# Performance work log

Measured on AMD Instinct MI355X. Metric: run time of the kernel, lower is better.

Reference implementation:

```python
import jax, jax.numpy as jnp
import numpy as np

N = 50000        # num nodes
E = 800000       # num edges (avg degree 16)
IN = 64          # in_channels
H = 128          # hidden_channels
C1 = 64          # Num_TCN (fine clusters)
C2 = 16          # Num_TCN2 (coarse clusters)
DROP = 0.5       # drop_rate
THRESH = 1.0 / (C1 - 1)  # default edge_pruning_threshold
LN_EPS = 1e-5


def layer_norm(x, g, b):
    mu = jnp.mean(x, axis=-1, keepdims=True)
    var = jnp.var(x, axis=-1, keepdims=True)
    return (x - mu) * jax.lax.rsqrt(var + LN_EPS) * g + b


def graph_conv(x_src, row, col, W_rel, b, W_root, num_nodes):
    # PyG GraphConv (aggr='add'): out = lin_rel(sum_{src->dst} x[src]) + lin_root(x)
    agg = jax.ops.segment_sum(x_src[row], col, num_segments=num_nodes)
    return agg @ W_rel.T + b + x_src @ W_root.T


def mincut_common(x, s, A_s, deg):
    # shared tail of sparse_mincut_pool given A_s = A @ s and degree vector
    C = s.shape[-1]
    pooled_x = s.T @ x                                   # [C, F]
    pooled_adj = s.T @ A_s                               # [C, C]
    mincut_num = jnp.trace(pooled_adj)
    mincut_den = jnp.trace(s.T @ (deg[:, None] * s)) + 1e-10
    mincut_loss = -mincut_num / mincut_den
    sTs = s.T @ s
    norm = jnp.linalg.norm(sTs)
    ortho_loss = jnp.linalg.norm(sTs / (norm + 1e-10) - jnp.eye(C, dtype=x.dtype) / jnp.sqrt(jnp.asarray(C, x.dtype)))
    adj = pooled_adj * (1.0 - jnp.eye(C, dtype=x.dtype))  # fill_diagonal_(0)
    d_sqrt_inv = 1.0 / (jnp.sqrt(adj.sum(axis=1)) + 1e-15)
    adj_norm = adj * d_sqrt_inv[:, None] * d_sqrt_inv[None, :]
    return pooled_x, adj_norm, mincut_loss, ortho_loss


def mincut_sparse(x, row, col, s_logits, num_nodes):
    s = jax.nn.softmax(s_logits, axis=-1)
    # A_s[row] += s[col]  (edge_weight = 1) -> [N, C] scatter-add
    A_s = jax.ops.segment_sum(s[col], row, num_segments=num_nodes)
    deg = jax.ops.segment_sum(jnp.ones((row.shape[0],), x.dtype), row, num_segments=num_nodes)
    return mincut_common(x, s, A_s, deg)


def mincut_dense(x, M, s_logits):
    # pooled graph: dense 0/1 adjacency M[i,j]; equivalent to edge list from nonzero(M)
    s = jax.nn.softmax(s_logits, axis=-1)
    A_s = M @ s
    deg = M.sum(axis=1)
    return mincut_common(x, s, A_s, deg)


def setup_inputs() -> dict:
    key = jax.random.key(0)
    ks = jax.random.split(key, 12)
    x = jax.random.normal(ks[0], (N, IN), jnp.float32)
    edge_index = jax.random.randint(ks[1], (2, E), 0, N, jnp.int32)
    # bernoulli(1 - drop_rate) node-drop mask, fixed for determinism
    drop_mask = (jax.random.uniform(ks[2], (N,)) > DROP).astype(jnp.float32)
    p = lambda k, shp: (jax.random.normal(k, shp, jnp.float32) * 0.05)
    return dict(
        x=x, edge_index=edge_index, drop_mask=drop_mask,
        W1_rel=p(ks[3], (H, IN)), b1=jnp.zeros((H,), jnp.float32), W1_root=p(ks[4], (H, IN)),
        pW1=p(ks[5], (C1, H)), pb1=jnp.zeros((C1,), jnp.float32),
        g1=jnp.ones((C1,), jnp.float32), be1=jnp.zeros((C1,), jnp.float32),
        W2_rel=p(ks[6], (H, H)), b2=jnp.zeros((H,), jnp.float32), W2_root=p(ks[7], (H, H)),
        pW2=p(ks[8], (C2, H)), pb2=jnp.zeros((C2,), jnp.float32),
        g2=jnp.ones((C2,), jnp.float32), be2=jnp.zeros((C2,), jnp.float32),
    )


def reference(x, edge_index, drop_mask, W1_rel, b1, W1_root, pW1, pb1, g1, be1,
              W2_rel, b2, W2_root, pW2, pb2, g2, be2):
    # training=True path, S=1 (loss sums / S are identity)
    row, col = edge_index[0], edge_index[1]
    x_drop = drop_mask[:, None] * x
    x1 = jax.nn.relu(graph_conv(x_drop, row, col, W1_rel, b1, W1_root, N))   # [N, H]
    s1 = layer_norm(x1 @ pW1.T + pb1, g1, be1)                               # [N, C1]
    ls1 = jax.nn.log_softmax(s1, axis=-1)
    x_pool1, adj_pool1, mc1, o1 = mincut_sparse(x1, row, col, s1, N)
    # edge pruning -> dense 0/1 pooled adjacency (replaces nonzero + edge list)
    M = jnp.where(adj_pool1 > THRESH, 1.0, 0.0).astype(x.dtype)              # [C1, C1]
    # GraphConv on pooled graph: aggregate x[src] at dst == M.T @ x_pool1
    x2 = jax.nn.relu((M.T @ x_pool1) @ W2_rel.T + b2 + x_pool1 @ W2_root.T)  # [C1, H]
    s2 = layer_norm(x2 @ pW2.T + pb2, g2, be2)                               # [C1, C2]
    ls2 = jax.nn.log_softmax(s2, axis=-1)
    _, _, mc2, o2 = mincut_dense(x2, M, s2)
    return (mc1, o1, mc2, o2, ls1, ls2)
```

## Files before the change

kernel.cpp:

```cpp
#include <hip/hip_runtime.h>
#include <hip/hip_bf16.h>
#include <hip/hip_fp16.h>

#define NN 50000
#define NE 800000
#define INC 64
#define HC 128
#define NC1 64
#define NC2 16
#define DCAP 64

#define OFF_FLAG 0
#define OFW_W1R 16
#define OFW_W1O 8208
#define OFW_B1  16400
#define OFW_PW1 16528
#define OFW_PB1 24720
#define OFW_G1  24784
#define OFW_BE1 24848
#define OFW_W2R 24912
#define OFW_B2  41296
#define OFW_W2O 41424
#define OFW_PW2 57808
#define OFW_PB2 59856
#define OFW_G2  59872
#define OFW_BE2 59888
#define CVT_TOTAL 59888

#define OFW_PW1T 59904
#define OFF_MG   68096
#define OFF_MTG  72192
#define OFF_DEG2 76288
#define OFF_S2G  76352
#define OFW_WCT  77376
#define OFF_XD   127792
#define OFF_X1   3327792
#define OFF_S    9727792
#define OFF_AGG  12927792
#define OFF_CSRC 16127792
#define OFF_SCAL 17727792
#define OFF_PX   17727808
#define OFF_PADJ 17736000
#define OFF_STS  17740096
#define OFF_CUR  17744192
#define OFF_Q    17794192
#define OFF_END  17844192
#define ZERO_FLOATS (OFF_END - OFF_SCAL)

#define OFF_PXSTSP OFF_XD
#define OFF_PADJP  OFF_X1
#define OFF_XD16   OFF_X1
#define OFF_S16    OFF_AGG
#define P_POOL 256
#define P_PADJ 1536
#define XSS 132

#define FC_G 2048
#define FC_SLICES (FC_G >> 3)
#define FC_ES ((NE + FC_SLICES - 1) / FC_SLICES)
#define FC_RANGE (NN >> 3)

__device__ inline float bflo(unsigned int u){ return __uint_as_float(u << 16); }
__device__ inline float bfhi(unsigned int u){ return __uint_as_float(u & 0xffff0000u); }

__device__ inline void store_out(void* out, long long idx, float v, bool bf){
  if (bf) ((__hip_bfloat16*)out)[idx] = __float2bfloat16(v);
  else    ((float*)out)[idx] = v;
}

__device__ inline float block_reduce_256(float v, float* red, int t){
  red[t] = v; __syncthreads();
#pragma unroll
  for (int sh = 128; sh > 0; sh >>= 1){
    if (t < sh) red[t] += red[t + sh];
    __syncthreads();
  }
  float r = red[0];
  __syncthreads();
  return r;
}

__global__ void k_detect(const unsigned int* __restrict__ dmw, float* __restrict__ flag){
  __shared__ int cnt;
  if (threadIdx.x == 0) cnt = 0;
  __syncthreads();
  int c = 0;
  for (int i = threadIdx.x; i < 12288; i += 256){
    unsigned int w = dmw[i];
    if (w == 0x3F803F80u || w == 0x00003F80u) c++;
  }
  atomicAdd(&cnt, c);
  __syncthreads();
  if (threadIdx.x == 0) flag[0] = (cnt > 64) ? 1.0f : 0.0f;
}

__global__ void k_cvt(const void* p0, const void* p1, const void* p2, const void* p3,
                      const void* p4, const void* p5, const void* p6, const void* p7,
                      const void* p8, const void* p9, const void* p10, const void* p11,
                      const void* p12, const void* p13,
                      const float* __restrict__ flag, float* __restrict__ ws){
  int i = blockIdx.x * blockDim.x + threadIdx.x;
  if (i >= CVT_TOTAL) return;
  const void* src; int off;
  if      (i < 8192 ){ src = p0;  off = i; }
  else if (i < 16384){ src = p1;  off = i - 8192; }
  else if (i < 16512){ src = p2;  off = i - 16384; }
  else if (i < 24704){ src = p3;  off = i - 16512; }
  else if (i < 24768){ src = p4;  off = i - 24704; }
  else if (i < 24832){ src = p5;  off = i - 24768; }
  else if (i < 24896){ src = p6;  off = i - 24832; }
  else if (i < 41280){ src = p7;  off = i - 24896; }
  else if (i < 41408){ src = p8;  off = i - 41280; }
  else if (i < 57792){ src = p9;  off = i - 41408; }
  else if (i < 59840){ src = p10; off = i - 57792; }
  else if (i < 59856){ src = p11; off = i - 59840; }
  else if (i < 59872){ src = p12; off = i - 59856; }
  else               { src = p13; off = i - 59872; }
  float v = (flag[0] > 0.5f) ? __bfloat162float(((const __hip_bfloat16*)src)[off])
                             : ((const float*)src)[off];
  ws[16 + i] = v;
  if (i < 8192){
    int h = i >> 6, j = i & 63;
    ws[OFW_WCT + j * 128 + h] = v;
  } else if (i < 16384){
    int o2 = i - 8192;
    int h = o2 >> 6, j = o2 & 63;
    ws[OFW_WCT + (64 + j) * 128 + h] = v;
  } else if (i >= 16512 && i < 24704){
    int o2 = i - 16512;
    int c = o2 >> 7, k = o2 & 127;
    ws[OFW_PW1T + k * 64 + c] = v;
  }
}

__global__ void k_xdrop(const void* __restrict__ xr, const void* __restrict__ dmr,
                        const float* __restrict__ flag, float* __restrict__ xd,
                        __half* __restrict__ xd16){
  int i4 = blockIdx.x * blockDim.x + threadIdx.x;
  if (i4 >= NN * 16) return;
  int n = i4 >> 4;
  float4 o;
  if (flag[0] > 0.5f){
    uint2 w = ((const uint2*)xr)[i4];
    float dv = __bfloat162float(((const __hip_bfloat16*)dmr)[n]);
    o.x = bflo(w.x) * dv; o.y = bfhi(w.x) * dv;
    o.z = bflo(w.y) * dv; o.w = bfhi(w.y) * dv;
  } else {
    float4 xv = ((const float4*)xr)[i4];
    float dv = ((const float*)dmr)[n];
    o.x = xv.x * dv; o.y = xv.y * dv; o.z = xv.z * dv; o.w = xv.w * dv;
  }
  ((float4*)xd)[i4] = o;
  __half2 ha = __floats2half2_rn(o.x, o.y);
  __half2 hb = __floats2half2_rn(o.z, o.w);
  uint2 hh;
  hh.x = *(unsigned int*)&ha;
  hh.y = *(unsigned int*)&hb;
  ((uint2*)xd16)[i4] = hh;
}

__global__ __launch_bounds__(256) void k_fillC(const int* __restrict__ ei, int* __restrict__ cur,
                        unsigned short* __restrict__ csrc2){
  int p = blockIdx.x & 7;
  int q = blockIdx.x >> 3;
  int lo = p * FC_RANGE;
  int base = q * FC_ES;
  int end = base + FC_ES; if (end > NE) end = NE;
  for (int e = base + (int)threadIdx.x; e < end; e += 256){
    int c = ei[NE + e];
    if ((unsigned)(c - lo) < (unsigned)FC_RANGE){
      int r = ei[e];
      int pos = atomicAdd(&cur[c], 1);
      if (pos < DCAP) csrc2[(c << 6) + pos] = (unsigned short)r;
    }
  }
}

#define G4ACC(Sq, Cq, Aq) \
    if (slot < Cq){ \
      uint2 u = *(const uint2*)(table + (Sq << 6) + (sub << 2)); \
      float2 f0 = __half22float2(*(__half2*)&u.x); \
      float2 f1 = __half22float2(*(__half2*)&u.y); \
      Aq.x += f0.x; Aq.y += f0.y; Aq.z += f1.x; Aq.w += f1.y; \
    }

__device__ inline void gather4h(const unsigned short* __restrict__ idx,
                                const int* __restrict__ cur,
                                int n0, const __half* __restrict__ table,
                                int lane, int g, int sub,
                                float4& A0, float4& A1, float4& A2, float4& A3){
  int c0 = cur[n0 + 0]; if (c0 > DCAP) c0 = DCAP;
  int c1 = cur[n0 + 1]; if (c1 > DCAP) c1 = DCAP;
  int c2 = cur[n0 + 2]; if (c2 > DCAP) c2 = DCAP;
  int c3 = cur[n0 + 3]; if (c3 > DCAP) c3 = DCAP;
  int my0 = (int)idx[((n0 + 0) << 6) + lane];
  int my1 = (int)idx[((n0 + 1) << 6) + lane];
  int my2 = (int)idx[((n0 + 2) << 6) + lane];
  int my3 = (int)idx[((n0 + 3) << 6) + lane];
  A0 = make_float4(0.f, 0.f, 0.f, 0.f); A1 = A0; A2 = A0; A3 = A0;
  int cmax = c0; if (c1 > cmax) cmax = c1; if (c2 > cmax) cmax = c2; if (c3 > cmax) cmax = c3;
#pragma unroll
  for (int i = 0; i < 4; ++i){
    int slot = g + (i << 2);
    int s0 = __shfl(my0, slot, 64);
    int s1 = __shfl(my1, slot, 64);
    int s2 = __shfl(my2, slot, 64);
    int s3 = __shfl(my3, slot, 64);
    G4ACC(s0, c0, A0)
    G4ACC(s1, c1, A1)
    G4ACC(s2, c2, A2)
    G4ACC(s3, c3, A3)
  }
  for (int i = 4; (i << 2) < cmax; ++i){
    int slot = g + (i << 2);
    int s0 = __shfl(my0, slot, 64);
    int s1 = __shfl(my1, slot, 64);
    int s2 = __shfl(my2, slot, 64);
    int s3 = __shfl(my3, slot, 64);
    G4ACC(s0, c0, A0)
    G4ACC(s1, c1, A1)
    G4ACC(s2, c2, A2)
    G4ACC(s3, c3, A3)
  }
}

__device__ inline void red4x(float4& A0, float4& A1, float4& A2, float4& A3){
#pragma unroll
  for (int o = 16; o < 64; o <<= 1){
    A0.x += __shfl_xor(A0.x, o, 64); A0.y += __shfl_xor(A0.y, o, 64);
    A0.z += __shfl_xor(A0.z, o, 64); A0.w += __shfl_xor(A0.w, o, 64);
    A1.x += __shfl_xor(A1.x, o, 64); A1.y += __shfl_xor(A1.y, o, 64);
    A1.z += __shfl_xor(A1.z, o, 64); A1.w += __shfl_xor(A1.w, o, 64);
    A2.x += __shfl_xor(A2.x, o, 64); A2.y += __shfl_xor(A2.y, o, 64);
    A2.z += __shfl_xor(A2.z, o, 64); A2.w += __shfl_xor(A2.w, o, 64);
    A3.x += __shfl_xor(A3.x, o, 64); A3.y += __shfl_xor(A3.y, o, 64);
    A3.z += __shfl_xor(A3.z, o, 64); A3.w += __shfl_xor(A3.w, o, 64);
  }
}

__global__ __launch_bounds__(256) void k_agg2(const int* __restrict__ cur,
                                              const unsigned short* __restrict__ csrc2,
                                              const __half* __restrict__ xd16,
                                              float* __restrict__ agg){
  int gid = blockIdx.x * 256 + threadIdx.x;
  int lane = gid & 63, wid = gid >> 6;
  int nw = (gridDim.x * 256) >> 6;
  int g = lane >> 4, sub = lane & 15;
  for (int nb = wid; nb < (NN >> 2); nb += nw){
    int n0 = nb << 2;
    float4 A0, A1, A2, A3;
    gather4h(csrc2, cur, n0, xd16, lane, g, sub, A0, A1, A2, A3);
    red4x(A0, A1, A2, A3);
    float4 W = (g == 0) ? A0 : (g == 1) ? A1 : (g == 2) ? A2 : A3;
    *(float4*)(agg + ((n0 + g) << 6) + (sub << 2)) = W;
  }
}

#define FMA4(ACC, AV) \
  ACC.x += AV.x*w0.x + AV.y*w1.x + AV.z*w2.x + AV.w*w3.x; \
  ACC.y += AV.x*w0.y + AV.y*w1.y + AV.z*w2.y + AV.w*w3.y; \
  ACC.z += AV.x*w0.z + AV.y*w1.z + AV.z*w2.z + AV.w*w3.z; \
  ACC.w += AV.x*w0.w + AV.y*w1.w + AV.z*w2.w + AV.w*w3.w;

__global__ __launch_bounds__(512, 2) void k_x1(const float* __restrict__ agg,
                                               const float* __restrict__ xd,
                                               const float* __restrict__ wts,
                                               float* __restrict__ x1){
  __shared__ __align__(16) float wt[128 * 128];
  __shared__ __align__(16) float at[64 * 128];
  int t = threadIdx.x;
  for (int f4 = t; f4 < 4096; f4 += 512)
    *(float4*)&wt[f4 << 2] = *(const float4*)&wts[OFW_WCT + (f4 << 2)];
  int ni = t >> 5;
  int cj = t & 31;
  float4 b4 = *(const float4*)&wts[OFW_B1 + (cj << 2)];
  const int ntiles = (NN + 63) >> 6;
  for (int tile = blockIdx.x; tile < ntiles; tile += gridDim.x){
    int base = tile << 6;
    __syncthreads();
    for (int f4 = t; f4 < 2048; f4 += 512){
      int i = f4 >> 5, kq = f4 & 31;
      int n = base + i;
      float4 v = make_float4(0.f, 0.f, 0.f, 0.f);
      if (n < NN){
        int k = kq << 2;
        v = (k < 64) ? *(const float4*)(agg + (n << 6) + k)
                     : *(const float4*)(xd  + (n << 6) + (k - 64));
      }
      *(float4*)&at[(i << 7) + (kq << 2)] = v;
    }
    __syncthreads();
    float4 acc0 = {0,0,0,0}, acc1 = {0,0,0,0}, acc2 = {0,0,0,0}, acc3 = {0,0,0,0};
    const float* ap = at + (ni << 9);
    const float* wp = wt + (cj << 2);
#pragma unroll 4
    for (int k = 0; k < 128; k += 4){
      float4 w0 = *(const float4*)(wp + ((k + 0) << 7));
      float4 w1 = *(const float4*)(wp + ((k + 1) << 7));
      float4 w2 = *(const float4*)(wp + ((k + 2) << 7));
      float4 w3 = *(const float4*)(wp + ((k + 3) << 7));
      float4 a0v = *(const float4*)(ap + k);
      float4 a1v = *(const float4*)(ap + 128 + k);
      float4 a2v = *(const float4*)(ap + 256 + k);
      float4 a3v = *(const float4*)(ap + 384 + k);
      FMA4(acc0, a0v)
      FMA4(acc1, a1v)
      FMA4(acc2, a2v)
      FMA4(acc3, a3v)
    }
    int n0 = base + (ni << 2);
    if (n0 + 0 < NN){
      float4 o; o.x = fmaxf(acc0.x + b4.x, 0.f); o.y = fmaxf(acc0.y + b4.y, 0.f);
      o.z = fmaxf(acc0.z + b4.z, 0.f); o.w = fmaxf(acc0.w + b4.w, 0.f);
      *(float4*)(x1 + (long long)(n0 + 0) * HC + (cj << 2)) = o;
    }
    if (n0 + 1 < NN){
      float4 o; o.x = fmaxf(acc1.x + b4.x, 0.f); o.y = fmaxf(acc1.y + b4.y, 0.f);
      o.z = fmaxf(acc1.z + b4.z, 0.f); o.w = fmaxf(acc1.w + b4.w, 0.f);
      *(float4*)(x1 + (long long)(n0 + 1) * HC + (cj << 2)) = o;
    }
    if (n0 + 2 < NN){
      float4 o; o.x = fmaxf(acc2.x + b4.x, 0.f); o.y = fmaxf(acc2.y + b4.y, 0.f);
      o.z = fmaxf(acc2.z + b4.z, 0.f); o.w = fmaxf(acc2.w + b4.w, 0.f);
      *(float4*)(x1 + (long long)(n0 + 2) * HC + (cj << 2)) = o;
    }
    if (n0 + 3 < NN){
      float4 o; o.x = fmaxf(acc3.x + b4.x, 0.f); o.y = fmaxf(acc3.y + b4.y, 0.f);
      o.z = fmaxf(acc3.z + b4.z, 0.f); o.w = fmaxf(acc3.w + b4.w, 0.f);
      *(float4*)(x1 + (long long)(n0 + 3) * HC + (cj << 2)) = o;
    }
  }
}

__global__ __launch_bounds__(256) void k_s1f(const float* __restrict__ x1,
                                             const float* __restrict__ wts,
                                             float* __restrict__ s,
                                             __half* __restrict__ s16,
                                             float* __restrict__ q,
                                             void* __restrict__ outp,
                                             const float* __restrict__ flag){
  __shared__ float xs[64 * XSS];
  __shared__ float pwc[64 * 64];
  __shared__ float gsh[64], bsh[64];
  int t = threadIdx.x;
  int base = blockIdx.x * 64;
  if (t < 64){ gsh[t] = wts[OFW_G1 + t]; bsh[t] = wts[OFW_BE1 + t]; }
  for (int f = t; f < 64 * 32; f += 256){
    int r = f >> 5, kq = f & 31;
    float4 v = (base + r < NN) ? *(const float4*)(x1 + (base + r) * HC + (kq << 2))
                               : make_float4(0, 0, 0, 0);
    *(float4*)&xs[r * XSS + (kq << 2)] = v;
  }
  int ni = t >> 4, cj = t & 15;
  float4 c0 = {0,0,0,0}, c1 = {0,0,0,0}, c2 = {0,0,0,0}, c3 = {0,0,0,0};
#pragma unroll
  for (int half = 0; half < 2; ++half){
    int k0 = half << 6;
    __syncthreads();
    for (int f = t; f < 1024; f += 256){
      int kk = f >> 4, qq = f & 15;
      *(float4*)&pwc[kk * 64 + (qq << 2)] =
          *(const float4*)&wts[OFW_PW1T + (k0 + kk) * 64 + (qq << 2)];
    }
    __syncthreads();
    for (int kk = 0; kk < 64; kk += 4){
      float4 a0 = *(const float4*)&xs[(ni * 4 + 0) * XSS + k0 + kk];
      float4 a1 = *(const float4*)&xs[(ni * 4 + 1) * XSS + k0 + kk];
      float4 a2 = *(const float4*)&xs[(ni * 4 + 2) * XSS + k0 + kk];
      float4 a3 = *(const float4*)&xs[(ni * 4 + 3) * XSS + k0 + kk];
      float4 b0 = *(const float4*)&pwc[(kk + 0) * 64 + (cj << 2)];
      float4 b1 = *(const float4*)&pwc[(kk + 1) * 64 + (cj << 2)];
      float4 b2 = *(const float4*)&pwc[(kk + 2) * 64 + (cj << 2)];
      float4 b3 = *(const float4*)&pwc[(kk + 3) * 64 + (cj << 2)];
      c0.x += a0.x*b0.x + a0.y*b1.x + a0.z*b2.x + a0.w*b3.x;
      c0.y += a0.x*b0.y + a0.y*b1.y + a0.z*b2.y + a0.w*b3.y;
      c0.z += a0.x*b0.z + a0.y*b1.z + a0.z*b2.z + a0.w*b3.z;
      c0.w += a0.x*b0.w + a0.y*b1.w + a0.z*b2.w + a0.w*b3.w;
      c1.x += a1.x*b0.x + a1.y*b1.x + a1.z*b2.x + a1.w*b3.x;
      c1.y += a1.x*b0.y + a1.y*b1.y + a1.z*b2.y + a1.w*b3.y;
      c1.z += a1.x*b0.z + a1.y*b1.z + a1.z*b2.z + a1.w*b3.z;
      c1.w += a1.x*b0.w + a1.y*b1.w + a1.z*b2.w + a1.w*b3.w;
      c2.x += a2.x*b0.x + a2.y*b1.x + a2.z*b2.x + a2.w*b3.x;
      c2.y += a2.x*b0.y + a2.y*b1.y + a2.z*b2.y + a2.w*b3.y;
      c2.z += a2.x*b0.z + a2.y*b1.z + a2.z*b2.z + a2.w*b3.z;
      c2.w += a2.x*b0.w + a2.y*b1.w + a2.z*b2.w + a2.w*b3.w;
      c3.x += a3.x*b0.x + a3.y*b1.x + a3.z*b2.x + a3.w*b3.x;
      c3.y += a3.x*b0.y + a3.y*b1.y + a3.z*b2.y + a3.w*b3.y;
      c3.z += a3.x*b0.z + a3.y*b1.z + a3.z*b2.z + a3.w*b3.z;
      c3.w += a3.x*b0.w + a3.y*b1.w + a3.z*b2.w + a3.w*b3.w;
    }
  }
  float4 pb = *(const float4*)&wts[OFW_PB1 + (cj << 2)];
  c0.x += pb.x; c0.y += pb.y; c0.z += pb.z; c0.w += pb.w;
  c1.x += pb.x; c1.y += pb.y; c1.z += pb.z; c1.w += pb.w;
  c2.x += pb.x; c2.y += pb.y; c2.z += pb.z; c2.w += pb.w;
  c3.x += pb.x; c3.y += pb.y; c3.z += pb.z; c3.w += pb.w;
  __syncthreads();
  *(float4*)&xs[(ni * 4 + 0) * XSS + (cj << 2)] = c0;
  *(float4*)&xs[(ni * 4 + 1) * XSS + (cj << 2)] = c1;
  *(float4*)&xs[(ni * 4 + 2) * XSS + (cj << 2)] = c2;
  *(float4*)&xs[(ni * 4 + 3) * XSS + (cj << 2)] = c3;
  __syncthreads();
  bool bf = flag[0] > 0.5f;
  int lane = t & 63, wv = t >> 6;
  float gl = gsh[lane], bl = bsh[lane];
  for (int rb = 0; rb < 16; rb += 4){
    int row = wv * 16 + rb;
    float z0 = xs[(row + 0) * XSS + lane];
    float z1 = xs[(row + 1) * XSS + lane];
    float z2 = xs[(row + 2) * XSS + lane];
    float z3 = xs[(row + 3) * XSS + lane];
    float s0 = z0, s1 = z1, s2 = z2, s3 = z3;
    float q0 = z0*z0, q1 = z1*z1, q2 = z2*z2, q3 = z3*z3;
#pragma unroll
    for (int o = 32; o > 0; o >>= 1){
      s0 += __shfl_xor(s0, o, 64); q0 += __shfl_xor(q0, o, 64);
      s1 += __shfl_xor(s1, o, 64); q1 += __shfl_xor(q1, o, 64);
      s2 += __shfl_xor(s2, o, 64); q2 += __shfl_xor(q2, o, 64);
      s3 += __shfl_xor(s3, o, 64); q3 += __shfl_xor(q3, o, 64);
    }
    float mu0 = s0 * 0.015625f, mu1 = s1 * 0.015625f;
    float mu2 = s2 * 0.015625f, mu3 = s3 * 0.015625f;
    float va0 = q0 * 0.015625f - mu0 * mu0;
    float va1 = q1 * 0.015625f - mu1 * mu1;
    float va2 = q2 * 0.015625f - mu2 * mu2;
    float va3 = q3 * 0.015625f - mu3 * mu3;
    float y0 = (z0 - mu0) * rsqrtf(va0 + 1e-5f) * gl + bl;
    float y1 = (z1 - mu1) * rsqrtf(va1 + 1e-5f) * gl + bl;
    float y2 = (z2 - mu2) * rsqrtf(va2 + 1e-5f) * gl + bl;
    float y3 = (z3 - mu3) * rsqrtf(va3 + 1e-5f) * gl + bl;
    float m0 = y0, m1 = y1, m2 = y2, m3 = y3;
#pragma unroll
    for (int o = 32; o > 0; o >>= 1){
      m0 = fmaxf(m0, __shfl_xor(m0, o, 64));
      m1 = fmaxf(m1, __shfl_xor(m1, o, 64));
      m2 = fmaxf(m2, __shfl_xor(m2, o, 64));
      m3 = fmaxf(m3, __shfl_xor(m3, o, 64));
    }
    float e0 = expf(y0 - m0), e1 = expf(y1 - m1);
    float e2 = expf(y2 - m2), e3 = expf(y3 - m3);
    float u0 = e0, u1 = e1, u2 = e2, u3 = e3;
    float w0 = e0*e0, w1 = e1*e1, w2 = e2*e2, w3 = e3*e3;
#pragma unroll
    for (int o = 32; o > 0; o >>= 1){
      u0 += __shfl_xor(u0, o, 64); w0 += __shfl_xor(w0, o, 64);
      u1 += __shfl_xor(u1, o, 64); w1 += __shfl_xor(w1, o, 64);
      u2 += __shfl_xor(u2, o, 64); w2 += __shfl_xor(w2, o, 64);
      u3 += __shfl_xor(u3, o, 64); w3 += __shfl_xor(w3, o, 64);
    }
    int n0 = base + row;
    if (n0 + 0 < NN){ float sv = e0 / u0; s[(n0 + 0) * 64 + lane] = sv;
      s16[(n0 + 0) * 64 + lane] = __float2half(sv);
      store_out(outp, 4LL + (long long)(n0 + 0) * 64 + lane, (y0 - m0) - logf(u0), bf);
      if (lane == 0) q[n0 + 0] = w0 / (u0 * u0); }
    if (n0 + 1 < NN){ float sv = e1 / u1; s[(n0 + 1) * 64 + lane] = sv;
      s16[(n0 + 1) * 64 + lane] = __float2half(sv);
      store_out(outp, 4LL + (long long)(n0 + 1) * 64 + lane, (y1 - m1) - logf(u1), bf);
      if (lane == 0) q[n0 + 1] = w1 / (u1 * u1); }
    if (n0 + 2 < NN){ float sv = e2 / u2; s[(n0 + 2) * 64 + lane] = sv;
      s16[(n0 + 2) * 64 + lane] = __float2half(sv);
      store_out(outp, 4LL + (long long)(n0 + 2) * 64 + lane, (y2 - m2) - logf(u2), bf);
      if (lane == 0) q[n0 + 2] = w2 / (u2 * u2); }
    if (n0 + 3 < NN){ float sv = e3 / u3; s[(n0 + 3) * 64 + lane] = sv;
      s16[(n0 + 3) * 64 + lane] = __float2half(sv);
      store_out(outp, 4LL + (long long)(n0 + 3) * 64 + lane, (y3 - m3) - logf(u3), bf);
      if (lane == 0) q[n0 + 3] = w3 / (u3 * u3); }
  }
}

__global__ __launch_bounds__(256) void k_den(const int* __restrict__ ei,
                                             const float* __restrict__ q,
                                             float* __restrict__ scal){
  __shared__ float red[256];
  int t = threadIdx.x;
  float acc = 0.0f;
  for (int e = blockIdx.x * 256 + t; e < NE; e += gridDim.x * 256)
    acc += q[ei[e]];
  float r = block_reduce_256(acc, red, t);
  if (t == 0) atomicAdd(&scal[0], r);
}

__global__ __launch_bounds__(256) void k_padj2(const int* __restrict__ cur,
                                               const unsigned short* __restrict__ csrc2,
                                               const __half* __restrict__ s16,
                                               const float* __restrict__ s,
                                               float* __restrict__ padjp){
  __shared__ float rs[16 * 64];
  __shared__ float ra[16 * 64];
  int t = threadIdx.x, lane = t & 63, w = t >> 6;
  int g = lane >> 4, sub = lane & 15;
  int i4 = t >> 4;
  int j4 = t & 15;
  float4 acc0 = {0,0,0,0}, acc1 = {0,0,0,0}, acc2 = {0,0,0,0}, acc3 = {0,0,0,0};
  const int nbatch = NN / 16;
  for (int b = blockIdx.x; b < nbatch; b += gridDim.x){
    int base = b * 16;
    int n0 = base + (w << 2);
    float4 A0, A1, A2, A3;
    gather4h(csrc2, cur, n0, s16, lane, g, sub, A0, A1, A2, A3);
    float4 R = *(const float4*)(s + ((n0 + g) << 6) + (sub << 2));
    red4x(A0, A1, A2, A3);
    float4 W = (g == 0) ? A0 : (g == 1) ? A1 : (g == 2) ? A2 : A3;
    int k = (w << 2) + g;
    *(float4*)&rs[k * 64 + (sub << 2)] = W;
    *(float4*)&ra[k * 64 + (sub << 2)] = R;
    __syncthreads();
#pragma unroll
    for (int kk = 0; kk < 16; ++kk){
      float4 a  = *(const float4*)&rs[kk * 64 + (i4 << 2)];
      float4 bv = *(const float4*)&ra[kk * 64 + (j4 << 2)];
      acc0.x += a.x * bv.x; acc0.y += a.x * bv.y; acc0.z += a.x * bv.z; acc0.w += a.x * bv.w;
      acc1.x += a.y * bv.x; acc1.y += a.y * bv.y; acc1.z += a.y * bv.z; acc1.w += a.y * bv.w;
      acc2.x += a.z * bv.x; acc2.y += a.z * bv.y; acc2.z += a.z * bv.z; acc2.w += a.z * bv.w;
      acc3.x += a.w * bv.x; acc3.y += a.w * bv.y; acc3.z += a.w * bv.z; acc3.w += a.w * bv.w;
    }
    __syncthreads();
  }
  float* pp = padjp + blockIdx.x * 4096;
  *(float4*)&pp[(i4 * 4 + 0) * 64 + (j4 << 2)] = acc0;
  *(float4*)&pp[(i4 * 4 + 1) * 64 + (j4 << 2)] = acc1;
  *(float4*)&pp[(i4 * 4 + 2) * 64 + (j4 << 2)] = acc2;
  *(float4*)&pp[(i4 * 4 + 3) * 64 + (j4 << 2)] = acc3;
}

__global__ __launch_bounds__(1024) void k_pool(const float* __restrict__ s,
                                               const float* __restrict__ x1,
                                               float* __restrict__ part){
  __shared__ float ssh[32 * 64];
  __shared__ float xsh[32 * 128];
  int t = threadIdx.x;
  int c = t >> 4, q = t & 15;
  float4 apx0 = {0,0,0,0}, apx1 = {0,0,0,0}, ast0 = {0,0,0,0};
  const int nbatch = (NN + 31) / 32;
  for (int b = blockIdx.x; b < nbatch; b += gridDim.x){
    int base = b * 32;
    int kmax = NN - base; if (kmax > 32) kmax = 32;
    if (t < 512){
      int k = t >> 4, col = t & 15;
      float4 v = (k < kmax) ? *(const float4*)(s + ((base + k) << 6) + (col << 2))
                            : make_float4(0, 0, 0, 0);
      *(float4*)&ssh[k * 64 + (col << 2)] = v;
    }
    {
      int k = t >> 5, col = t & 31;
      float4 v = (k < kmax) ? *(const float4*)(x1 + (base + k) * HC + (col << 2))
                            : make_float4(0, 0, 0, 0);
      *(float4*)&xsh[k * 128 + (col << 2)] = v;
    }
    __syncthreads();
    for (int k = 0; k < kmax; ++k){
      float sv = ssh[k * 64 + c];
      float4 xv0 = *(const float4*)&xsh[k * 128 + (q << 2)];
      float4 xv1 = *(const float4*)&xsh[k * 128 + ((q + 16) << 2)];
      float4 s0  = *(const float4*)&ssh[k * 64 + (q << 2)];
      apx0.x += sv * xv0.x; apx0.y += sv * xv0.y; apx0.z += sv * xv0.z; apx0.w += sv * xv0.w;
      apx1.x += sv * xv1.x; apx1.y += sv * xv1.y; apx1.z += sv * xv1.z; apx1.w += sv * xv1.w;
      ast0.x += sv * s0.x;  ast0.y += sv * s0.y;  ast0.z += sv * s0.z;  ast0.w += sv * s0.w;
    }
    __syncthreads();
  }
  float* pp = part + blockIdx.x * 12288;
  *(float4*)&pp[c * 128 + (q << 2)]        = apx0;
  *(float4*)&pp[c * 128 + ((q + 16) << 2)] = apx1;
  *(float4*)&pp[8192 + c * 64 + (q << 2)]  = ast0;
}

__global__ __launch_bounds__(256) void k_red(const float* __restrict__ pxstsp,
                                             const float* __restrict__ padjp,
                                             float* __restrict__ px,
                                             float* __restrict__ sts,
                                             float* __restrict__ padj){
  __shared__ float sh[256];
  int b = blockIdx.x, t = threadIdx.x;
  int ci = t & 63, pc = t >> 6;
  if (b < 192){
    int cell = b * 64 + ci;
    float a0 = 0, a1 = 0, a2 = 0, a3 = 0;
    const float* basep = pxstsp + cell;
    int p0 = pc * (P_POOL / 4);
    for (int p = 0; p < P_POOL / 4; p += 4){
      a0 += basep[(p0 + p    ) * 12288];
      a1 += basep[(p0 + p + 1) * 12288];
      a2 += basep[(p0 + p + 2) * 12288];
      a3 += basep[(p0 + p + 3) * 12288];
    }
    sh[t] = (a0 + a1) + (a2 + a3);
    __syncthreads();
    if (t < 64){
      float r = sh[t] + sh[t + 64] + sh[t + 128] + sh[t + 192];
      int cell2 = b * 64 + t;
      if (cell2 < 8192) px[cell2] = r; else sts[cell2 - 8192] = r;
    }
  } else {
    int cell = (b - 192) * 64 + ci;
    float a0 = 0, a1 = 0, a2 = 0, a3 = 0;
    const float* basep = padjp + cell;
    int p0 = pc * (P_PADJ / 4);
    for (int p = 0; p < P_PADJ / 4; p += 4){
      a0 += basep[(p0 + p    ) * 4096];
      a1 += basep[(p0 + p + 1) * 4096];
      a2 += basep[(p0 + p + 2) * 4096];
      a3 += basep[(p0 + p + 3) * 4096];
    }
    sh[t] = (a0 + a1) + (a2 + a3);
    __syncthreads();
    if (t < 64) padj[(b - 192) * 64 + t] = sh[t] + sh[t + 64] + sh[t + 128] + sh[t + 192];
  }
}

__global__ __launch_bounds__(256) void k_m(const float* __restrict__ padj,
                                           const float* __restrict__ sts,
                                           float* __restrict__ Mg,
                                           float* __restrict__ Mtg,
                                           float* __restrict__ deg2,
                                           float* __restrict__ scal){
  __shared__ float red[256];
  __shared__ float psh[4096];
  __shared__ float dsi[64];
  int t = threadIdx.x;
  const float TH = 1.0f / 63.0f;
  for (int i = t; i < 4096; i += 256) psh[i] = padj[i];
  __syncthreads();
  float v = (t < 64) ? psh[t * 65] : 0.0f;
  float num1 = block_reduce_256(v, red, t);
  v = 0.0f;
  for (int i = t; i < 4096; i += 256){ float e = sts[i]; v += e * e; }
  float nrm1 = sqrtf(block_reduce_256(v, red, t));
  v = 0.0f;
  for (int i = t; i < 4096; i += 256){
    float e = sts[i] / (nrm1 + 1e-10f) - ((i % 65 == 0) ? 0.125f : 0.0f);
    v += e * e;
  }
  float o1 = sqrtf(block_reduce_256(v, red, t));
  if (t < 64){
    float rs = 0.0f;
    for (int j = 0; j < 64; ++j) rs += (j == t) ? 0.0f : psh[t * 64 + j];
    dsi[t] = 1.0f / (sqrtf(rs) + 1e-15f);
  }
  __syncthreads();
  for (int i = t; i < 4096; i += 256){
    int r = i >> 6, c = i & 63;
    float a = (r == c) ? 0.0f : psh[i];
    float m = (a * dsi[r] * dsi[c] > TH) ? 1.0f : 0.0f;
    Mg[i] = m;
    Mtg[c * 64 + r] = m;
  }
  __syncthreads();
  for (int i = t; i < 4096; i += 256){
    int r = i >> 6, c = i & 63;
    float a = (r == c) ? 0.0f : psh[i];
    psh[i] = (a * dsi[r] * dsi[c] > TH) ? 1.0f : 0.0f;
  }
  __syncthreads();
  if (t < 64){
    float d2 = 0.0f;
    for (int j = 0; j < 64; ++j) d2 += psh[t * 64 + j];
    deg2[t] = d2;
  }
  if (t == 0){ scal[1] = num1; scal[2] = o1; }
}

__global__ __launch_bounds__(128) void k_x2(const float* __restrict__ Mtg,
                                            const float* __restrict__ px,
                                            const float* __restrict__ wts,
                                            float* __restrict__ s2g,
                                            void* __restrict__ out,
                                            const float* __restrict__ flag){
  __shared__ float mt[64], pxc[128], mpsh[128], x2sh[128];
  __shared__ float part[16][9], lsh[16], stat[2];
  int c = blockIdx.x, t = threadIdx.x;
  if (t < 64) mt[t] = Mtg[c * 64 + t];
  pxc[t] = px[c * 128 + t];
  __syncthreads();
  float mp = 0.0f;
  for (int i = 0; i < 64; ++i) mp += mt[i] * px[i * 128 + t];
  mpsh[t] = mp;
  __syncthreads();
  float acc = wts[OFW_B2 + t];
  const float* wrr = wts + OFW_W2R + t * 128;
  const float* wor = wts + OFW_W2O + t * 128;
  for (int k = 0; k < 128; ++k) acc += mpsh[k] * wrr[k] + pxc[k] * wor[k];
  x2sh[t] = fmaxf(acc, 0.0f);
  __syncthreads();
  { int u = t >> 3, p = t & 7;
    const float* pw = wts + OFW_PW2 + u * 128 + p * 16;
    float pa = 0.0f;
    for (int k = 0; k < 16; ++k) pa += x2sh[p * 16 + k] * pw[k];
    part[u][p] = pa;
  }
  __syncthreads();
  if (t < 16){
    float l = wts[OFW_PB2 + t];
    for (int p = 0; p < 8; ++p) l += part[t][p];
    lsh[t] = l;
  }
  __syncthreads();
  if (t == 0){
    float mu = 0.0f;
    for (int u = 0; u < 16; ++u) mu += lsh[u];
    mu *= (1.0f / 16.0f);
    float var = 0.0f;
    for (int u = 0; u < 16; ++u){ float d = lsh[u] - mu; var += d * d; }
    var *= (1.0f / 16.0f);
    float rstd = rsqrtf(var + 1e-5f);
    float m = -3.4e38f;
    for (int u = 0; u < 16; ++u){
      lsh[u] = (lsh[u] - mu) * rstd * wts[OFW_G2 + u] + wts[OFW_BE2 + u];
      m = fmaxf(m, lsh[u]);
    }
    float se = 0.0f;
    for (int u = 0; u < 16; ++u) se += expf(lsh[u] - m);
    stat[0] = m; stat[1] = logf(se);
  }
  __syncthreads();
  if (t < 16){
    float ls = (lsh[t] - stat[0]) - stat[1];
    store_out(out, 4LL + (long long)NN * NC1 + c * 16 + t, ls, flag[0] > 0.5f);
    s2g[c * 16 + t] = expf(ls);
  }
}

__global__ __launch_bounds__(256) void k_tail(const float* __restrict__ Mg,
                                              const float* __restrict__ s2g,
                                              const float* __restrict__ deg2,
                                              const float* __restrict__ scal,
                                              void* __restrict__ out,
                                              const float* __restrict__ flag){
  __shared__ float red[256];
  __shared__ float Msh[4096];
  __shared__ float s2sh[1024];
  __shared__ float d2sh[64];
  __shared__ float sts2[256];
  int t = threadIdx.x;
  for (int i = t; i < 4096; i += 256) Msh[i] = Mg[i];
  for (int i = t; i < 1024; i += 256) s2sh[i] = s2g[i];
  if (t < 64) d2sh[t] = deg2[t];
  __syncthreads();
  float vnum = 0.0f, vden = 0.0f;
  for (int m = 0; m < 4; ++m){
    int id = t + m * 256;
    int c = id >> 4, u = id & 15;
    float a = 0.0f;
    for (int j = 0; j < 64; ++j) a += Msh[c * 64 + j] * s2sh[j * 16 + u];
    float sv = s2sh[id];
    vnum += sv * a;
    vden += d2sh[c] * sv * sv;
  }
  float num2 = block_reduce_256(vnum, red, t);
  float den2 = block_reduce_256(vden, red, t) + 1e-10f;
  { int u = t >> 4, w = t & 15;
    float a = 0.0f;
    for (int c2 = 0; c2 < 64; ++c2) a += s2sh[c2 * 16 + u] * s2sh[c2 * 16 + w];
    sts2[t] = a;
  }
  __syncthreads();
  float v = sts2[t] * sts2[t];
  float nrm2 = sqrtf(block_reduce_256(v, red, t));
  { float e = sts2[t] / (nrm2 + 1e-10f) - (((t >> 4) == (t & 15)) ? 0.25f : 0.0f);
    v = e * e; }
  float o2 = sqrtf(block_reduce_256(v, red, t));
  if (t == 0){
    bool bf = flag[0] > 0.5f;
    float den = scal[0] + 1e-10f;
    store_out(out, 0, -scal[1] / den, bf);
    store_out(out, 1, scal[2], bf);
    store_out(out, 2, -num2 / den2, bf);
    store_out(out, 3, o2, bf);
  }
}

extern "C" void kernel_launch(void* const* d_in, const int* in_sizes, int n_in,
                              void* d_out, int out_size, void* d_ws, size_t ws_size,
                              hipStream_t stream){
  const void* x  = d_in[0];
  const int*  ei = (const int*)d_in[1];
  const void* dm = d_in[2];

  float* ws    = (float*)d_ws;
  float* flag  = ws + OFF_FLAG;
  float* xd    = ws + OFF_XD;
  float* x1    = ws + OFF_X1;
  float* s     = ws + OFF_S;
  float* agg   = ws + OFF_AGG;
  float* px    = ws + OFF_PX;
  float* padj  = ws + OFF_PADJ;
  float* sts   = ws + OFF_STS;
  float* scal  = ws + OFF_SCAL;
  float* Mg    = ws + OFF_MG;
  float* Mtg   = ws + OFF_MTG;
  float* deg2  = ws + OFF_DEG2;
  float* s2g   = ws + OFF_S2G;
  float* q     = ws + OFF_Q;
  float* pxstsp= ws + OFF_PXSTSP;
  float* padjp = ws + OFF_PADJP;
  __half* xd16 = (__half*)(ws + OFF_XD16);
  __half* s16  = (__half*)(ws + OFF_S16);
  unsigned short* csrc2 = (unsigned short*)(ws + OFF_CSRC);
  int* cur = (int*)(ws + OFF_CUR);

  hipMemsetAsync(ws + OFF_SCAL, 0, (size_t)ZERO_FLOATS * sizeof(float), stream);

  k_detect<<<1, 256, 0, stream>>>((const unsigned int*)dm, flag);
  k_cvt<<<(CVT_TOTAL + 255) / 256, 256, 0, stream>>>(
      d_in[3], d_in[5], d_in[4], d_in[6], d_in[7], d_in[8], d_in[9],
      d_in[10], d_in[11], d_in[12], d_in[13], d_in[14], d_in[15], d_in[16],
      flag, ws);
  k_xdrop<<<(NN * 16 + 255) / 256, 256, 0, stream>>>(x, dm, flag, xd, xd16);
  k_fillC<<<FC_G, 256, 0, stream>>>(ei, cur, csrc2);
  k_agg2<<<2048, 256, 0, stream>>>(cur, csrc2, xd16, agg);
  k_x1<<<256, 512, 0, stream>>>(agg, xd, ws, x1);
  k_s1f<<<(NN + 63) / 64, 256, 0, stream>>>(x1, ws, s, s16, q, d_out, flag);
  k_den<<<256, 256, 0, stream>>>(ei, q, scal);
  k_pool<<<P_POOL, 1024, 0, stream>>>(s, x1, pxstsp);
  k_padj2<<<P_PADJ, 256, 0, stream>>>(cur, csrc2, s16, s, padjp);
  k_red<<<256, 256, 0, stream>>>(pxstsp, padjp, px, sts, padj);
  k_m<<<1, 256, 0, stream>>>(padj, sts, Mg, Mtg, deg2, scal);
  k_x2<<<64, 128, 0, stream>>>(Mtg, px, ws, s2g, d_out, flag);
  k_tail<<<1, 256, 0, stream>>>(Mg, s2g, deg2, scal, d_out, flag);
}
```

Before: 393.2 us.

## Split s1 projection from layernorm-softmax and drop fp32 soft assignment buffer

The fused projection+layernorm+softmax kernel becomes two kernels. One is a persistent GEMM that keeps the whole projection weight in shared memory and writes logits. The other does the row-wise layernorm, softmax and log-softmax one wave per row group. The fp32 copy of s is no longer written, and the pooling and pooled-adjacency kernels read the fp16 s16 instead. This cuts global writes and reads of a 50000x64 fp32 array and raises GEMM occupancy, at the cost of an extra round trip for the fp32 logits and reduced precision in the pooled sums. The layernorm kernel also assumes NN is a multiple of 4 and drops per-row bounds checks.

```diff
diff --git a/kernel.cpp b/kernel.cpp
--- a/kernel.cpp
+++ b/kernel.cpp
@@ -47,6 +47,7 @@
 #define OFF_END  17844192
 #define ZERO_FLOATS (OFF_END - OFF_SCAL)
 
+#define OFF_LOG    OFF_XD
 #define OFF_PXSTSP OFF_XD
 #define OFF_PADJP  OFF_X1
 #define OFF_XD16   OFF_X1
@@ -332,84 +333,80 @@
   }
 }
 
-__global__ __launch_bounds__(256) void k_s1f(const float* __restrict__ x1,
-                                             const float* __restrict__ wts,
-                                             float* __restrict__ s,
-                                             __half* __restrict__ s16,
-                                             float* __restrict__ q,
-                                             void* __restrict__ outp,
-                                             const float* __restrict__ flag){
-  __shared__ float xs[64 * XSS];
-  __shared__ float pwc[64 * 64];
-  __shared__ float gsh[64], bsh[64];
+__global__ __launch_bounds__(512, 2) void k_s1g(const float* __restrict__ x1,
+                                                const float* __restrict__ wts,
+                                                float* __restrict__ logit){
+  __shared__ __align__(16) float pw[128 * 64];
+  __shared__ __align__(16) float at[64 * 128];
   int t = threadIdx.x;
-  int base = blockIdx.x * 64;
-  if (t < 64){ gsh[t] = wts[OFW_G1 + t]; bsh[t] = wts[OFW_BE1 + t]; }
-  for (int f = t; f < 64 * 32; f += 256){
-    int r = f >> 5, kq = f & 31;
-    float4 v = (base + r < NN) ? *(const float4*)(x1 + (base + r) * HC + (kq << 2))
-                               : make_float4(0, 0, 0, 0);
-    *(float4*)&xs[r * XSS + (kq << 2)] = v;
-  }
-  int ni = t >> 4, cj = t & 15;
-  float4 c0 = {0,0,0,0}, c1 = {0,0,0,0}, c2 = {0,0,0,0}, c3 = {0,0,0,0};
-#pragma unroll
-  for (int half = 0; half < 2; ++half){
-    int k0 = half << 6;
-    __syncthreads();
-    for (int f = t; f < 1024; f += 256){
-      int kk = f >> 4, qq = f & 15;
-      *(float4*)&pwc[kk * 64 + (qq << 2)] =
-          *(const float4*)&wts[OFW_PW1T + (k0 + kk) * 64 + (qq << 2)];
-    }
-    __syncthreads();
-    for (int kk = 0; kk < 64; kk += 4){
-      float4 a0 = *(const float4*)&xs[(ni * 4 + 0) * XSS + k0 + kk];
-      float4 a1 = *(const float4*)&xs[(ni * 4 + 1) * XSS + k0 + kk];
-      float4 a2 = *(const float4*)&xs[(ni * 4 + 2) * XSS + k0 + kk];
-      float4 a3 = *(const float4*)&xs[(ni * 4 + 3) * XSS + k0 + kk];
-      float4 b0 = *(const float4*)&pwc[(kk + 0) * 64 + (cj << 2)];
-      float4 b1 = *(const float4*)&pwc[(kk + 1) * 64 + (cj << 2)];
-      float4 b2 = *(const float4*)&pwc[(kk + 2) * 64 + (cj << 2)];
-      float4 b3 = *(const float4*)&pwc[(kk + 3) * 64 + (cj << 2)];
-      c0.x += a0.x*b0.x + a0.y*b1.x + a0.z*b2.x + a0.w*b3.x;
-      c0.y += a0.x*b0.y + a0.y*b1.y + a0.z*b2.y + a0.w*b3.y;
-      c0.z += a0.x*b0.z + a0.y*b1.z + a0.z*b2.z + a0.w*b3.z;
-      c0.w += a0.x*b0.w + a0.y*b1.w + a0.z*b2.w + a0.w*b3.w;
-      c1.x += a1.x*b0.x + a1.y*b1.x + a1.z*b2.x + a1.w*b3.x;
-      c1.y += a1.x*b0.y + a1.y*b1.y + a1.z*b2.y + a1.w*b3.y;
-      c1.z += a1.x*b0.z + a1.y*b1.z + a1.z*b2.z + a1.w*b3.z;
-      c1.w += a1.x*b0.w + a1.y*b1.w + a1.z*b2.w + a1.w*b3.w;
-      c2.x += a2.x*b0.x + a2.y*b1.x + a2.z*b2.x + a2.w*b3.x;
-      c2.y += a2.x*b0.y + a2.y*b1.y + a2.z*b2.y + a2.w*b3.y;
-      c2.z += a2.x*b0.z + a2.y*b1.z + a2.z*b2.z + a2.w*b3.z;
-      c2.w += a2.x*b0.w + a2.y*b1.w + a2.z*b2.w + a2.w*b3.w;
-      c3.x += a3.x*b0.x + a3.y*b1.x + a3.z*b2.x + a3.w*b3.x;
-      c3.y += a3.x*b0.y + a3.y*b1.y + a3.z*b2.y + a3.w*b3.y;
-      c3.z += a3.x*b0.z + a3.y*b1.z + a3.z*b2.z + a3.w*b3.z;
-      c3.w += a3.x*b0.w + a3.y*b1.w + a3.z*b2.w + a3.w*b3.w;
-    }
-  }
-  float4 pb = *(const float4*)&wts[OFW_PB1 + (cj << 2)];
-  c0.x += pb.x; c0.y += pb.y; c0.z += pb.z; c0.w += pb.w;
-  c1.x += pb.x; c1.y += pb.y; c1.z += pb.z; c1.w += pb.w;
-  c2.x += pb.x; c2.y += pb.y; c2.z += pb.z; c2.w += pb.w;
-  c3.x += pb.x; c3.y += pb.y; c3.z += pb.z; c3.w += pb.w;
-  __syncthreads();
-  *(float4*)&xs[(ni * 4 + 0) * XSS + (cj << 2)] = c0;
-  *(float4*)&xs[(ni * 4 + 1) * XSS + (cj << 2)] = c1;
-  *(float4*)&xs[(ni * 4 + 2) * XSS + (cj << 2)] = c2;
-  *(float4*)&xs[(ni * 4 + 3) * XSS + (cj << 2)] = c3;
-  __syncthreads();
+  for (int f4 = t; f4 < 2048; f4 += 512)
+    *(float4*)&pw[f4 << 2] = *(const float4*)&wts[OFW_PW1T + (f4 << 2)];
+  int ni = t >> 5;
+  int cj = t & 31;
+  float2 pb = *(const float2*)&wts[OFW_PB1 + (cj << 1)];
+  const int ntiles = (NN + 63) >> 6;
+  for (int tile = blockIdx.x; tile < ntiles; tile += gridDim.x){
+    int base = tile << 6;
+    __syncthreads();
+    for (int f4 = t; f4 < 2048; f4 += 512){
+      int i = f4 >> 5, kq = f4 & 31;
+      int n = base + i;
+      float4 v = (n < NN) ? *(const float4*)(x1 + (long long)n * HC + (kq << 2))
+                          : make_float4(0.f, 0.f, 0.f, 0.f);
+      *(float4*)&at[(i << 7) + (kq << 2)] = v;
+    }
+    __syncthreads();
+    float2 a0 = {0,0}, a1 = {0,0}, a2 = {0,0}, a3 = {0,0};
+    const float* ap = at + (ni << 9);
+    const float* wp = pw + (cj << 1);
+#pragma unroll 4
+    for (int k = 0; k < 128; k += 4){
+      float2 w0 = *(const float2*)(wp + ((k + 0) << 6));
+      float2 w1 = *(const float2*)(wp + ((k + 1) << 6));
+      float2 w2 = *(const float2*)(wp + ((k + 2) << 6));
+      float2 w3 = *(const float2*)(wp + ((k + 3) << 6));
+      float4 x0 = *(const float4*)(ap + k);
+      float4 x1v = *(const float4*)(ap + 128 + k);
+      float4 x2v = *(const float4*)(ap + 256 + k);
+      float4 x3v = *(const float4*)(ap + 384 + k);
+      a0.x += x0.x*w0.x + x0.y*w1.x + x0.z*w2.x + x0.w*w3.x;
+      a0.y += x0.x*w0.y + x0.y*w1.y + x0.z*w2.y + x0.w*w3.y;
+      a1.x += x1v.x*w0.x + x1v.y*w1.x + x1v.z*w2.x + x1v.w*w3.x;
+      a1.y += x1v.x*w0.y + x1v.y*w1.y + x1v.z*w2.y + x1v.w*w3.y;
+      a2.x += x2v.x*w0.x + x2v.y*w1.x + x2v.z*w2.x + x2v.w*w3.x;
+      a2.y += x2v.x*w0.y + x2v.y*w1.y + x2v.z*w2.y + x2v.w*w3.y;
+      a3.x += x3v.x*w0.x + x3v.y*w1.x + x3v.z*w2.x + x3v.w*w3.x;
+      a3.y += x3v.x*w0.y + x3v.y*w1.y + x3v.z*w2.y + x3v.w*w3.y;
+    }
+    int n0 = base + (ni << 2);
+    if (n0 + 0 < NN){ float2 o; o.x = a0.x + pb.x; o.y = a0.y + pb.y;
+      *(float2*)(logit + (long long)(n0 + 0) * 64 + (cj << 1)) = o; }
+    if (n0 + 1 < NN){ float2 o; o.x = a1.x + pb.x; o.y = a1.y + pb.y;
+      *(float2*)(logit + (long long)(n0 + 1) * 64 + (cj << 1)) = o; }
+    if (n0 + 2 < NN){ float2 o; o.x = a2.x + pb.x; o.y = a2.y + pb.y;
+      *(float2*)(logit + (long long)(n0 + 2) * 64 + (cj << 1)) = o; }
+    if (n0 + 3 < NN){ float2 o; o.x = a3.x + pb.x; o.y = a3.y + pb.y;
+      *(float2*)(logit + (long long)(n0 + 3) * 64 + (cj << 1)) = o; }
+  }
+}
+
+__global__ __launch_bounds__(256) void k_lnsm(const float* __restrict__ logit,
+                                              const float* __restrict__ wts,
+                                              __half* __restrict__ s16,
+                                              float* __restrict__ q,
+                                              void* __restrict__ outp,
+                                              const float* __restrict__ flag){
+  int t = threadIdx.x;
+  int lane = t & 63, wv = t >> 6;
   bool bf = flag[0] > 0.5f;
-  int lane = t & 63, wv = t >> 6;
-  float gl = gsh[lane], bl = bsh[lane];
-  for (int rb = 0; rb < 16; rb += 4){
-    int row = wv * 16 + rb;
-    float z0 = xs[(row + 0) * XSS + lane];
-    float z1 = xs[(row + 1) * XSS + lane];
-    float z2 = xs[(row + 2) * XSS + lane];
-    float z3 = xs[(row + 3) * XSS + lane];
+  float gl = wts[OFW_G1 + lane], bl = wts[OFW_BE1 + lane];
+  int wg = blockIdx.x * 4 + wv;
+  int nw = gridDim.x * 4;
+  for (int r = wg * 4; r < NN; r += nw * 4){
+    float z0 = logit[(long long)(r + 0) * 64 + lane];
+    float z1 = logit[(long long)(r + 1) * 64 + lane];
+    float z2 = logit[(long long)(r + 2) * 64 + lane];
+    float z3 = logit[(long long)(r + 3) * 64 + lane];
     float s0 = z0, s1 = z1, s2 = z2, s3 = z3;
     float q0 = z0*z0, q1 = z1*z1, q2 = z2*z2, q3 = z3*z3;
 #pragma unroll
@@ -448,23 +445,20 @@
       u2 += __shfl_xor(u2, o, 64); w2 += __shfl_xor(w2, o, 64);
       u3 += __shfl_xor(u3, o, 64); w3 += __shfl_xor(w3, o, 64);
     }
-    int n0 = base + row;
-    if (n0 + 0 < NN){ float sv = e0 / u0; s[(n0 + 0) * 64 + lane] = sv;
-      s16[(n0 + 0) * 64 + lane] = __float2half(sv);
-      store_out(outp, 4LL + (long long)(n0 + 0) * 64 + lane, (y0 - m0) - logf(u0), bf);
-      if (lane == 0) q[n0 + 0] = w0 / (u0 * u0); }
-    if (n0 + 1 < NN){ float sv = e1 / u1; s[(n0 + 1) * 64 + lane] = sv;
-      s16[(n0 + 1) * 64 + lane] = __float2half(sv);
-      store_out(outp, 4LL + (long long)(n0 + 1) * 64 + lane, (y1 - m1) - logf(u1), bf);
-      if (lane == 0) q[n0 + 1] = w1 / (u1 * u1); }
-    if (n0 + 2 < NN){ float sv = e2 / u2; s[(n0 + 2) * 64 + lane] = sv;
-      s16[(n0 + 2) * 64 + lane] = __float2half(sv);
-      store_out(outp, 4LL + (long long)(n0 + 2) * 64 + lane, (y2 - m2) - logf(u2), bf);
-      if (lane == 0) q[n0 + 2] = w2 / (u2 * u2); }
-    if (n0 + 3 < NN){ float sv = e3 / u3; s[(n0 + 3) * 64 + lane] = sv;
-      s16[(n0 + 3) * 64 + lane] = __float2half(sv);
-      store_out(outp, 4LL + (long long)(n0 + 3) * 64 + lane, (y3 - m3) - logf(u3), bf);
-      if (lane == 0) q[n0 + 3] = w3 / (u3 * u3); }
+    s16[(long long)(r + 0) * 64 + lane] = __float2half(e0 / u0);
+    s16[(long long)(r + 1) * 64 + lane] = __float2half(e1 / u1);
+    s16[(long long)(r + 2) * 64 + lane] = __float2half(e2 / u2);
+    s16[(long long)(r + 3) * 64 + lane] = __float2half(e3 / u3);
+    store_out(outp, 4LL + (long long)(r + 0) * 64 + lane, (y0 - m0) - logf(u0), bf);
+    store_out(outp, 4LL + (long long)(r + 1) * 64 + lane, (y1 - m1) - logf(u1), bf);
+    store_out(outp, 4LL + (long long)(r + 2) * 64 + lane, (y2 - m2) - logf(u2), bf);
+    store_out(outp, 4LL + (long long)(r + 3) * 64 + lane, (y3 - m3) - logf(u3), bf);
+    if (lane == 0){
+      q[r + 0] = w0 / (u0 * u0);
+      q[r + 1] = w1 / (u1 * u1);
+      q[r + 2] = w2 / (u2 * u2);
+      q[r + 3] = w3 / (u3 * u3);
+    }
   }
 }
 
@@ -483,7 +477,6 @@
 __global__ __launch_bounds__(256) void k_padj2(const int* __restrict__ cur,
                                                const unsigned short* __restrict__ csrc2,
                                                const __half* __restrict__ s16,
-                                               const float* __restrict__ s,
                                                float* __restrict__ padjp){
   __shared__ float rs[16 * 64];
   __shared__ float ra[16 * 64];
@@ -498,7 +491,9 @@
     int n0 = base + (w << 2);
     float4 A0, A1, A2, A3;
     gather4h(csrc2, cur, n0, s16, lane, g, sub, A0, A1, A2, A3);
-    float4 R = *(const float4*)(s + ((n0 + g) << 6) + (sub << 2));
+    uint2 ru = *(const uint2*)(s16 + ((n0 + g) << 6) + (sub << 2));
+    float2 rf0 = __half22float2(*(__half2*)&ru.x), rf1 = __half22float2(*(__half2*)&ru.y);
+    float4 R = make_float4(rf0.x, rf0.y, rf1.x, rf1.y);
     red4x(A0, A1, A2, A3);
     float4 W = (g == 0) ? A0 : (g == 1) ? A1 : (g == 2) ? A2 : A3;
     int k = (w << 2) + g;
@@ -523,7 +518,7 @@
   *(float4*)&pp[(i4 * 4 + 3) * 64 + (j4 << 2)] = acc3;
 }
 
-__global__ __launch_bounds__(1024) void k_pool(const float* __restrict__ s,
+__global__ __launch_bounds__(1024) void k_pool(const __half* __restrict__ s16,
                                                const float* __restrict__ x1,
                                                float* __restrict__ part){
   __shared__ float ssh[32 * 64];
@@ -537,8 +532,12 @@
     int kmax = NN - base; if (kmax > 32) kmax = 32;
     if (t < 512){
       int k = t >> 4, col = t & 15;
-      float4 v = (k < kmax) ? *(const float4*)(s + ((base + k) << 6) + (col << 2))
-                            : make_float4(0, 0, 0, 0);
+      float4 v = make_float4(0.f, 0.f, 0.f, 0.f);
+      if (k < kmax){
+        uint2 u = *(const uint2*)(s16 + ((base + k) << 6) + (col << 2));
+        float2 f0 = __half22float2(*(__half2*)&u.x), f1 = __half22float2(*(__half2*)&u.y);
+        v = make_float4(f0.x, f0.y, f1.x, f1.y);
+      }
       *(float4*)&ssh[k * 64 + (col << 2)] = v;
     }
     {
@@ -780,7 +779,6 @@
   float* flag  = ws + OFF_FLAG;
   float* xd    = ws + OFF_XD;
   float* x1    = ws + OFF_X1;
-  float* s     = ws + OFF_S;
   float* agg   = ws + OFF_AGG;
   float* px    = ws + OFF_PX;
   float* padj  = ws + OFF_PADJ;
@@ -791,6 +789,7 @@
   float* deg2  = ws + OFF_DEG2;
   float* s2g   = ws + OFF_S2G;
   float* q     = ws + OFF_Q;
+  float* logit = ws + OFF_LOG;
   float* pxstsp= ws + OFF_PXSTSP;
   float* padjp = ws + OFF_PADJP;
   __half* xd16 = (__half*)(ws + OFF_XD16);
@@ -809,10 +808,11 @@
   k_fillC<<<FC_G, 256, 0, stream>>>(ei, cur, csrc2);
   k_agg2<<<2048, 256, 0, stream>>>(cur, csrc2, xd16, agg);
   k_x1<<<256, 512, 0, stream>>>(agg, xd, ws, x1);
-  k_s1f<<<(NN + 63) / 64, 256, 0, stream>>>(x1, ws, s, s16, q, d_out, flag);
+  k_s1g<<<512, 512, 0, stream>>>(x1, ws, logit);
+  k_lnsm<<<1024, 256, 0, stream>>>(logit, ws, s16, q, d_out, flag);
   k_den<<<256, 256, 0, stream>>>(ei, q, scal);
-  k_pool<<<P_POOL, 1024, 0, stream>>>(s, x1, pxstsp);
-  k_padj2<<<P_PADJ, 256, 0, stream>>>(cur, csrc2, s16, s, padjp);
+  k_pool<<<P_POOL, 1024, 0, stream>>>(s16, x1, pxstsp);
+  k_padj2<<<P_PADJ, 256, 0, stream>>>(cur, csrc2, s16, padjp);
   k_red<<<256, 256, 0, stream>>>(pxstsp, padjp, px, sts, padj);
   k_m<<<1, 256, 0, stream>>>(padj, sts, Mg, Mtg, deg2, scal);
   k_x2<<<64, 128, 0, stream>>>(Mtg, px, ws, s2g, d_out, flag);
```

Measured after the change: 388.5 us. About the same (-1.2%).
